# Optimization experiments

Measured on AMD Instinct MI355X. Metric: run time of the kernel, lower is better.

Reference implementation:

```python
import jax, jax.numpy as jnp
import numpy as np

NUM_HEADS = 16
GROUP_NUM = 4
HIDDEN = 1024
HEAD_DIM = HIDDEN // NUM_HEADS
EPS = 1e-5


def layernorm(x, g, b):
    mu = jnp.mean(x, axis=-1, keepdims=True)
    var = jnp.var(x, axis=-1, keepdims=True)
    return (x - mu) * jax.lax.rsqrt(var + EPS) * g + b


def setup_inputs() -> dict:
    key = jax.random.key(0)
    ks = jax.random.split(key, 12)
    s = 0.02
    return {
        "hidden_state": jax.random.normal(ks[0], (2, 2048, HIDDEN), jnp.float32),
        "wq": jax.random.normal(ks[1], (HIDDEN, HIDDEN), jnp.float32) * s,
        "bq": jnp.zeros((HIDDEN,), jnp.float32),
        "wk": jax.random.normal(ks[2], (GROUP_NUM * HEAD_DIM, HIDDEN), jnp.float32) * s,
        "bk": jnp.zeros((GROUP_NUM * HEAD_DIM,), jnp.float32),
        "wv": jax.random.normal(ks[3], (GROUP_NUM * HEAD_DIM, HIDDEN), jnp.float32) * s,
        "bv": jnp.zeros((GROUP_NUM * HEAD_DIM,), jnp.float32),
        "wo": jax.random.normal(ks[4], (HIDDEN, HIDDEN), jnp.float32) * s,
        "bo": jnp.zeros((HIDDEN,), jnp.float32),
        "ln_g": jnp.ones((HIDDEN,), jnp.float32),
        "ln_b": jnp.zeros((HIDDEN,), jnp.float32),
        "w1": jax.random.normal(ks[5], (HIDDEN, HIDDEN), jnp.float32) * s,
        "b1": jnp.zeros((HIDDEN,), jnp.float32),
        "w2": jax.random.normal(ks[6], (HIDDEN, HIDDEN), jnp.float32) * s,
        "b2": jnp.zeros((HIDDEN,), jnp.float32),
        "fln_g": jnp.ones((HIDDEN,), jnp.float32),
        "fln_b": jnp.zeros((HIDDEN,), jnp.float32),
    }


def reference(hidden_state, wq, bq, wk, bk, wv, bv, wo, bo, ln_g, ln_b,
              w1, b1, w2, b2, fln_g, fln_b):
    B, S, H = hidden_state.shape
    hpg = NUM_HEADS // GROUP_NUM  # heads per KV group

    q = hidden_state @ wq.T + bq  # [B,S,H]
    k = hidden_state @ wk.T + bk  # [B,S,G*D]
    v = hidden_state @ wv.T + bv

    q = q.reshape(B, S, NUM_HEADS, HEAD_DIM).transpose(0, 2, 1, 3)      # [B,Hh,S,D]
    k = k.reshape(B, S, GROUP_NUM, HEAD_DIM).transpose(0, 2, 1, 3)      # [B,G,S,D]
    v = v.reshape(B, S, GROUP_NUM, HEAD_DIM).transpose(0, 2, 1, 3)
    # expand KV groups to full head count (consecutive repeat, matching torch expand+reshape)
    k = jnp.repeat(k, hpg, axis=1)  # [B,Hh,S,D]
    v = jnp.repeat(v, hpg, axis=1)

    scale = 1.0 / jnp.sqrt(jnp.float32(HEAD_DIM))
    scores = jnp.einsum('bhsd,bhtd->bhst', q, k) * scale  # [B,Hh,S,S]
    probs = jax.nn.softmax(scores, axis=-1)
    attn = jnp.einsum('bhst,bhtd->bhsd', probs, v)  # [B,Hh,S,D]

    # Faithful to source: transpose(-1,-2) then raw flat view to [B, S, Hh*D]
    attn = jnp.swapaxes(attn, -1, -2).reshape(B, -1, HEAD_DIM * NUM_HEADS)

    out = layernorm(hidden_state + attn @ wo.T + bo, ln_g, ln_b)
    ffn = out @ w1.T + b1
    ffn = jax.nn.relu(ffn) @ w2.T + b2
    return layernorm(out + ffn, fln_g, fln_b)
```

## Files before the change

kernel.cpp:

```cpp
#include <hip/hip_runtime.h>
#include <math.h>

#define HIDDEN 1024
#define SEQ 2048

typedef __attribute__((ext_vector_type(8))) short short8;
typedef __attribute__((ext_vector_type(4))) float f32x4;

__device__ __forceinline__ unsigned short f2bf(float x) {
  union { float f; unsigned u; } c; c.f = x;
  unsigned r = c.u + 0x7FFFu + ((c.u >> 16) & 1u);
  return (unsigned short)(r >> 16);
}
__device__ __forceinline__ float bf2f(unsigned short h) {
  union { unsigned u; float f; } c; c.u = ((unsigned)h) << 16;
  return c.f;
}

__device__ __forceinline__ float fexp2(float x) {
  float r; asm("v_exp_f32 %0, %1" : "=v"(r) : "v"(x)); return r;
}

__device__ __forceinline__ unsigned cvt_pk_bf16(float lo, float hi) {
  unsigned r;
  asm("v_cvt_pk_bf16_f32 %0, %1, %2" : "=v"(r) : "v"(lo), "v"(hi));
  return r;
}

__device__ __forceinline__ void async_copy16(const void* g, void* l) {
  __builtin_amdgcn_global_load_lds(
      (const __attribute__((address_space(1))) unsigned int*)g,
      (__attribute__((address_space(3))) unsigned int*)l, 16, 0, 0);
}

__global__ __launch_bounds__(256) void cvt_all(
    const float* __restrict__ hs, const float* __restrict__ wq,
    const float* __restrict__ wk, const float* __restrict__ wv,
    const float* __restrict__ wo, const float* __restrict__ w1,
    const float* __restrict__ w2,
    unsigned short* __restrict__ hsb, unsigned short* __restrict__ wqb,
    unsigned short* __restrict__ wkb, unsigned short* __restrict__ wvb,
    unsigned short* __restrict__ wob, unsigned short* __restrict__ w1b,
    unsigned short* __restrict__ w2b)
{
  const int i = blockIdx.x * 256 + threadIdx.x;
  const float* src; unsigned short* dst; int off;
  if (i < 1048576)      { src = hs; dst = hsb; off = i; }
  else if (i < 1310720) { src = wq; dst = wqb; off = i - 1048576; }
  else if (i < 1376256) { src = wk; dst = wkb; off = i - 1310720; }
  else if (i < 1441792) { src = wv; dst = wvb; off = i - 1376256; }
  else if (i < 1703936) { src = wo; dst = wob; off = i - 1441792; }
  else if (i < 1966080) { src = w1; dst = w1b; off = i - 1703936; }
  else                  { src = w2; dst = w2b; off = i - 1966080; }
  float4 v = ((const float4*)src)[off];
  ushort4 o;
  o.x = f2bf(v.x); o.y = f2bf(v.y); o.z = f2bf(v.z); o.w = f2bf(v.w);
  ((ushort4*)dst)[off] = o;
}

template<bool RELU>
__global__ __launch_bounds__(256) void gemm_mfma(
    const unsigned short* __restrict__ A, const unsigned short* __restrict__ W,
    const float* __restrict__ bias, unsigned short* __restrict__ C,
    int M, int N, int K)
{
  __shared__ unsigned short As[64 * 64];
  __shared__ unsigned short Bs[64 * 64];
  const int tid = threadIdx.x;
  const int lane = tid & 63, wave = tid >> 6;
  const int ln = lane & 15, quad = lane >> 4;
  const int wm = (wave >> 1) * 32, wn = (wave & 1) * 32;

  const int flat = blockIdx.x;
  const int swz = (flat & 7) * ((int)gridDim.x >> 3) + (flat >> 3);
  const int ntx = N >> 6;
  const int m0 = (swz / ntx) * 64, n0 = (swz % ntx) * 64;

  f32x4 acc[2][2];
#pragma unroll
  for (int i = 0; i < 2; ++i)
#pragma unroll
    for (int j = 0; j < 2; ++j) acc[i][j] = (f32x4){0.f, 0.f, 0.f, 0.f};

  for (int k0 = 0; k0 < K; k0 += 64) {
#pragma unroll
    for (int it = 0; it < 2; ++it) {
      const int c = (wave * 2 + it) * 64 + lane;
      const int row = c >> 3, gc = (c & 7) ^ (row & 7);
      async_copy16(A + (size_t)(m0 + row) * K + k0 + gc * 8,
                   &As[(wave * 2 + it) * 512]);
      async_copy16(W + (size_t)(n0 + row) * K + k0 + gc * 8,
                   &Bs[(wave * 2 + it) * 512]);
    }
    __syncthreads();

    short8 af[2][2], bfr[2][2];
#pragma unroll
    for (int i = 0; i < 2; ++i) {
      const int row = wm + i * 16 + ln;
#pragma unroll
      for (int f = 0; f < 2; ++f) {
        const int ch = row * 8 + ((f * 4 + quad) ^ (row & 7));
        af[i][f] = *(const short8*)&As[ch * 8];
      }
    }
#pragma unroll
    for (int j = 0; j < 2; ++j) {
      const int row = wn + j * 16 + ln;
#pragma unroll
      for (int f = 0; f < 2; ++f) {
        const int ch = row * 8 + ((f * 4 + quad) ^ (row & 7));
        bfr[j][f] = *(const short8*)&Bs[ch * 8];
      }
    }
#pragma unroll
    for (int i = 0; i < 2; ++i)
#pragma unroll
      for (int j = 0; j < 2; ++j) {
        acc[i][j] = __builtin_amdgcn_mfma_f32_16x16x32_bf16(af[i][0], bfr[j][0], acc[i][j], 0, 0, 0);
        acc[i][j] = __builtin_amdgcn_mfma_f32_16x16x32_bf16(af[i][1], bfr[j][1], acc[i][j], 0, 0, 0);
      }
    __syncthreads();
  }

#pragma unroll
  for (int j = 0; j < 2; ++j) {
    const int n = n0 + wn + j * 16 + ln;
    const float bv = bias[n];
#pragma unroll
    for (int i = 0; i < 2; ++i) {
#pragma unroll
      for (int rr = 0; rr < 4; ++rr) {
        const int m = m0 + wm + i * 16 + quad * 4 + rr;
        float v = acc[i][j][rr] + bv;
        if (RELU) v = fmaxf(v, 0.f);
        C[(size_t)m * N + n] = f2bf(v);
      }
    }
  }
}

__global__ __launch_bounds__(256) void gemm_qkv(
    const unsigned short* __restrict__ A,
    const unsigned short* __restrict__ Wq, const unsigned short* __restrict__ Wk,
    const unsigned short* __restrict__ Wv,
    const float* __restrict__ bq, const float* __restrict__ bk,
    const float* __restrict__ bv,
    unsigned short* __restrict__ Qo, unsigned short* __restrict__ Ko,
    unsigned short* __restrict__ Vt)
{
  __shared__ unsigned short As[64 * 64];
  __shared__ unsigned short Bs[128 * 64];

  const int flat = blockIdx.x;
  const int swz = (flat & 7) * 96 + (flat >> 3);
  const int bx = swz % 12, by = swz / 12;

  int mode, nw0;
  const unsigned short* W;
  const float* bias;
  if (bx < 8)       { mode = 0; W = Wq; bias = bq; nw0 = bx * 128; }
  else if (bx < 10) { mode = 1; W = Wk; bias = bk; nw0 = (bx - 8) * 128; }
  else              { mode = 2; W = Wv; bias = bv; nw0 = (bx - 10) * 128; }

  const int tid = threadIdx.x;
  const int lane = tid & 63, wave = tid >> 6;
  const int ln = lane & 15, quad = lane >> 4;
  const int wm = (wave >> 1) * 32, wn = (wave & 1) * 64;
  const int m0 = by * 64;
  const int K = 1024;

  f32x4 acc[2][4];
#pragma unroll
  for (int i = 0; i < 2; ++i)
#pragma unroll
    for (int j = 0; j < 4; ++j) acc[i][j] = (f32x4){0.f, 0.f, 0.f, 0.f};

  for (int k0 = 0; k0 < K; k0 += 64) {
#pragma unroll
    for (int it = 0; it < 2; ++it) {
      const int c = (wave * 2 + it) * 64 + lane;
      const int row = c >> 3, gc = (c & 7) ^ (row & 7);
      async_copy16(A + (size_t)(m0 + row) * K + k0 + gc * 8,
                   &As[(wave * 2 + it) * 512]);
    }
#pragma unroll
    for (int it = 0; it < 4; ++it) {
      const int c = (wave * 4 + it) * 64 + lane;
      const int row = c >> 3, gc = (c & 7) ^ (row & 7);
      async_copy16(W + (size_t)(nw0 + row) * K + k0 + gc * 8,
                   &Bs[(wave * 4 + it) * 512]);
    }
    __syncthreads();

    short8 af[2][2], bfr[4][2];
#pragma unroll
    for (int i = 0; i < 2; ++i) {
      const int row = wm + i * 16 + ln;
#pragma unroll
      for (int f = 0; f < 2; ++f) {
        const int ch = row * 8 + ((f * 4 + quad) ^ (row & 7));
        af[i][f] = *(const short8*)&As[ch * 8];
      }
    }
#pragma unroll
    for (int j = 0; j < 4; ++j) {
      const int row = wn + j * 16 + ln;
#pragma unroll
      for (int f = 0; f < 2; ++f) {
        const int ch = row * 8 + ((f * 4 + quad) ^ (row & 7));
        bfr[j][f] = *(const short8*)&Bs[ch * 8];
      }
    }
#pragma unroll
    for (int i = 0; i < 2; ++i)
#pragma unroll
      for (int j = 0; j < 4; ++j) {
        acc[i][j] = __builtin_amdgcn_mfma_f32_16x16x32_bf16(af[i][0], bfr[j][0], acc[i][j], 0, 0, 0);
        acc[i][j] = __builtin_amdgcn_mfma_f32_16x16x32_bf16(af[i][1], bfr[j][1], acc[i][j], 0, 0, 0);
      }
    __syncthreads();
  }

#pragma unroll
  for (int j = 0; j < 4; ++j) {
    const int nl = nw0 + wn + j * 16 + ln;
    const float bvv = bias[nl];
#pragma unroll
    for (int i = 0; i < 2; ++i) {
#pragma unroll
      for (int rr = 0; rr < 4; ++rr) {
        const int m = m0 + wm + i * 16 + quad * 4 + rr;
        const float v = acc[i][j][rr] + bvv;
        if (mode == 0) {
          Qo[(size_t)m * 1024 + nl] = f2bf(v);
        } else if (mode == 1) {
          Ko[(size_t)m * 256 + nl] = f2bf(v);
        } else {
          const int b = m >> 11, s = m & 2047;
          Vt[((size_t)b * 256 + nl) * SEQ + s] = f2bf(v);
        }
      }
    }
  }
}

__global__ __launch_bounds__(256) void attn_mfma(
    const unsigned short* __restrict__ Q, const unsigned short* __restrict__ Kb,
    const unsigned short* __restrict__ Vt,
    unsigned short* __restrict__ N0, unsigned short* __restrict__ N1,
    float* __restrict__ LS)
{
  __shared__ unsigned short Ks[2][64 * 64];
  __shared__ unsigned short Vs[2][64 * 64];

  const int hwb = blockIdx.x;
  const int swz = (hwb & 7) * 64 + (hwb >> 3);
  const int qblk = swz & 7, half = (swz >> 3) & 1, h = (swz >> 4) & 15, b = swz >> 8;
  const int g = h >> 2;

  unsigned short* __restrict__ numO = half ? N1 : N0;
  float* __restrict__ lsO = LS + half * 65536;

  const int tid = threadIdx.x, lane = tid & 63, wave = tid >> 6;
  const int ln = lane & 15, quad = lane >> 4, q8 = quad * 8;
  const int s0 = qblk * 256;
  const float qscale = 0.125f * 1.44269504f;

  const int ln7 = ln & 7;
  const int x0 = (quad ^ ln7) * 8;
  const int x1 = ((4 + quad) ^ ln7) * 8;

  short8 ones;
#pragma unroll
  for (int e = 0; e < 8; ++e) ones[e] = (short)0x3F80;

  short8 qf[4][2];
#pragma unroll
  for (int qg = 0; qg < 4; ++qg) {
    const unsigned short* qsrc =
        Q + ((size_t)(b * SEQ + s0 + wave * 64 + qg * 16 + ln)) * 1024 + h * 64 + q8;
    qf[qg][0] = *(const short8*)qsrc;
    qf[qg][1] = *(const short8*)(qsrc + 32);
#pragma unroll
    for (int e = 0; e < 8; ++e) {
      qf[qg][0][e] = (short)f2bf(bf2f((unsigned short)qf[qg][0][e]) * qscale);
      qf[qg][1][e] = (short)f2bf(bf2f((unsigned short)qf[qg][1][e]) * qscale);
    }
  }

  const int srow = lane >> 3;
  const int sgcc = (lane & 7) ^ srow;

  auto stage = [&](int t0, int p) {
#pragma unroll
    for (int it = 0; it < 2; ++it) {
      const int row = wave * 16 + it * 8 + srow;
      const int skey = (row & 32) | ((row & 8) << 1) | ((row & 4) << 1) |
                       ((row & 16) >> 2) | (row & 3);
      async_copy16(Kb + (size_t)(b * SEQ + t0 + skey) * 256 + g * 64 + sgcc * 8,
                   &Ks[p][(wave * 2 + it) * 512]);
      async_copy16(Vt + (size_t)(b * 256 + g * 64 + row) * SEQ + t0 + sgcc * 8,
                   &Vs[p][(wave * 2 + it) * 512]);
    }
  };

  f32x4 of[4][4];
  f32x4 ls[4];
#pragma unroll
  for (int qg = 0; qg < 4; ++qg) {
    ls[qg] = (f32x4){0.f, 0.f, 0.f, 0.f};
#pragma unroll
    for (int jd = 0; jd < 4; ++jd) of[qg][jd] = (f32x4){0.f, 0.f, 0.f, 0.f};
  }

  const int tbase = half * 16;
  stage(tbase * 64, 0);

  for (int tt = 0; tt < 16; ++tt) {
    const int p = tt & 1;
    if (tt < 15) {
      stage((tbase + tt + 1) * 64, p ^ 1);
      asm volatile("s_waitcnt vmcnt(4)" ::: "memory");
    } else {
      asm volatile("s_waitcnt vmcnt(0)" ::: "memory");
    }
    __builtin_amdgcn_s_barrier();
    asm volatile("" ::: "memory");

    f32x4 sc[4][4];
#pragma unroll
    for (int jn = 0; jn < 4; ++jn) {
      const int krow = (jn * 16 + ln) * 64;
      const short8 kf0 = *(const short8*)&Ks[p][krow + x0];
      const short8 kf1 = *(const short8*)&Ks[p][krow + x1];
#pragma unroll
      for (int qg = 0; qg < 4; ++qg) {
        f32x4 z = (f32x4){0.f, 0.f, 0.f, 0.f};
        z = __builtin_amdgcn_mfma_f32_16x16x32_bf16(kf0, qf[qg][0], z, 0, 0, 0);
        z = __builtin_amdgcn_mfma_f32_16x16x32_bf16(kf1, qf[qg][1], z, 0, 0, 0);
        sc[qg][jn] = z;
      }
    }

    short8 pf[4][2];
#pragma unroll
    for (int qg = 0; qg < 4; ++qg) {
#pragma unroll
      for (int jn = 0; jn < 4; ++jn)
#pragma unroll
        for (int r = 0; r < 4; ++r) sc[qg][jn][r] = fexp2(sc[qg][jn][r]);
#pragma unroll
      for (int F = 0; F < 2; ++F) {
        union { unsigned u[4]; short8 s; } pk;
        pk.u[0] = cvt_pk_bf16(sc[qg][2 * F][0], sc[qg][2 * F][1]);
        pk.u[1] = cvt_pk_bf16(sc[qg][2 * F][2], sc[qg][2 * F][3]);
        pk.u[2] = cvt_pk_bf16(sc[qg][2 * F + 1][0], sc[qg][2 * F + 1][1]);
        pk.u[3] = cvt_pk_bf16(sc[qg][2 * F + 1][2], sc[qg][2 * F + 1][3]);
        pf[qg][F] = pk.s;
      }
      ls[qg] = __builtin_amdgcn_mfma_f32_16x16x32_bf16(pf[qg][0], ones, ls[qg], 0, 0, 0);
      ls[qg] = __builtin_amdgcn_mfma_f32_16x16x32_bf16(pf[qg][1], ones, ls[qg], 0, 0, 0);
    }

#pragma unroll
    for (int jd = 0; jd < 4; ++jd) {
      const int vrow = (jd * 16 + ln) * 64;
      const short8 vf0 = *(const short8*)&Vs[p][vrow + x0];
      const short8 vf1 = *(const short8*)&Vs[p][vrow + x1];
#pragma unroll
      for (int qg = 0; qg < 4; ++qg) {
        of[qg][jd] = __builtin_amdgcn_mfma_f32_16x16x32_bf16(pf[qg][0], vf0, of[qg][jd], 0, 0, 0);
        of[qg][jd] = __builtin_amdgcn_mfma_f32_16x16x32_bf16(pf[qg][1], vf1, of[qg][jd], 0, 0, 0);
      }
    }

    asm volatile("" ::: "memory");
    __builtin_amdgcn_s_barrier();
    asm volatile("" ::: "memory");
  }

#pragma unroll
  for (int qg = 0; qg < 4; ++qg) {
    const int sbase = s0 + wave * 64 + qg * 16 + quad * 4;
    if (ln == 0) {
#pragma unroll
      for (int r = 0; r < 4; ++r)
        lsO[(b * 16 + h) * 2048 + sbase + r] = ls[qg][r];
    }
#pragma unroll
    for (int jd = 0; jd < 4; ++jd) {
      const int d = jd * 16 + ln;
      ushort4 ov;
      ov.x = f2bf(of[qg][jd][0]);
      ov.y = f2bf(of[qg][jd][1]);
      ov.z = f2bf(of[qg][jd][2]);
      ov.w = f2bf(of[qg][jd][3]);
      *(ushort4*)&numO[((size_t)b * 1024 + h * 64 + d) * SEQ + sbase] = ov;
    }
  }
}

__global__ __launch_bounds__(256) void attn_reduce(
    const unsigned short* __restrict__ N0, unsigned short* att,
    const float* __restrict__ LS)
{
  const int i = (blockIdx.x * 256 + threadIdx.x) * 4;
  const int row = i >> 11, s = i & 2047;
  const int h = (row >> 6) & 15, b = row >> 10;
  const int lsi = (b * 16 + h) * 2048 + s;
  const float4 l0 = *(const float4*)&LS[lsi];
  const float4 l1 = *(const float4*)&LS[65536 + lsi];
  const ushort4 a = *(const ushort4*)&N0[i];
  const ushort4 c = *(const ushort4*)&att[i];
  ushort4 o;
  o.x = f2bf((bf2f(a.x) + bf2f(c.x)) / (l0.x + l1.x));
  o.y = f2bf((bf2f(a.y) + bf2f(c.y)) / (l0.y + l1.y));
  o.z = f2bf((bf2f(a.z) + bf2f(c.z)) / (l0.z + l1.z));
  o.w = f2bf((bf2f(a.w) + bf2f(c.w)) / (l0.w + l1.w));
  *(ushort4*)&att[i] = o;
}

__device__ __forceinline__ void ln_core(float x[4], const float* gam, const float* bet,
                                        int tid, float out[4]) {
  float s1 = x[0] + x[1] + x[2] + x[3];
  float s2 = x[0] * x[0] + x[1] * x[1] + x[2] * x[2] + x[3] * x[3];
#pragma unroll
  for (int off = 1; off < 64; off <<= 1) {
    s1 += __shfl_xor(s1, off);
    s2 += __shfl_xor(s2, off);
  }
  __shared__ float r1[4], r2[4];
  const int wave = tid >> 6;
  if ((tid & 63) == 0) { r1[wave] = s1; r2[wave] = s2; }
  __syncthreads();
  s1 = r1[0] + r1[1] + r1[2] + r1[3];
  s2 = r2[0] + r2[1] + r2[2] + r2[3];
  const float mu  = s1 * (1.0f / HIDDEN);
  const float var = s2 * (1.0f / HIDDEN) - mu * mu;
  const float inv = rsqrtf(var + 1e-5f);
  float4 gv = *(const float4*)&gam[tid * 4];
  float4 bv = *(const float4*)&bet[tid * 4];
  out[0] = (x[0] - mu) * inv * gv.x + bv.x;
  out[1] = (x[1] - mu) * inv * gv.y + bv.y;
  out[2] = (x[2] - mu) * inv * gv.z + bv.z;
  out[3] = (x[3] - mu) * inv * gv.w + bv.w;
}

__global__ __launch_bounds__(256) void resid_ln1(
    const float* __restrict__ X, const unsigned short* __restrict__ Y,
    const float* __restrict__ gam, const float* __restrict__ bet,
    unsigned short* __restrict__ outb)
{
  const int row = blockIdx.x, tid = threadIdx.x;
  const size_t base = (size_t)row * HIDDEN + tid * 4;
  float4 a = *(const float4*)&X[base];
  ushort4 yv = *(const ushort4*)&Y[base];
  float x[4] = {a.x + bf2f(yv.x), a.y + bf2f(yv.y), a.z + bf2f(yv.z), a.w + bf2f(yv.w)};
  float o[4];
  ln_core(x, gam, bet, tid, o);
  ushort4 ov;
  ov.x = f2bf(o[0]); ov.y = f2bf(o[1]); ov.z = f2bf(o[2]); ov.w = f2bf(o[3]);
  *(ushort4*)&outb[base] = ov;
}

__global__ __launch_bounds__(256) void resid_ln2(
    const unsigned short* __restrict__ X, const unsigned short* __restrict__ Y,
    const float* __restrict__ gam, const float* __restrict__ bet,
    float* __restrict__ out)
{
  const int row = blockIdx.x, tid = threadIdx.x;
  const size_t base = (size_t)row * HIDDEN + tid * 4;
  ushort4 xv = *(const ushort4*)&X[base];
  ushort4 yv = *(const ushort4*)&Y[base];
  float x[4] = {bf2f(xv.x) + bf2f(yv.x), bf2f(xv.y) + bf2f(yv.y),
                bf2f(xv.z) + bf2f(yv.z), bf2f(xv.w) + bf2f(yv.w)};
  float o[4];
  ln_core(x, gam, bet, tid, o);
  float4 ov; ov.x = o[0]; ov.y = o[1]; ov.z = o[2]; ov.w = o[3];
  *(float4*)&out[base] = ov;
}

extern "C" void kernel_launch(void* const* d_in, const int* in_sizes, int n_in,
                              void* d_out, int out_size, void* d_ws, size_t ws_size,
                              hipStream_t stream)
{
  (void)in_sizes; (void)n_in; (void)out_size; (void)ws_size;
  const float* hs  = (const float*)d_in[0];
  const float* wq  = (const float*)d_in[1];
  const float* bq  = (const float*)d_in[2];
  const float* wk  = (const float*)d_in[3];
  const float* bk  = (const float*)d_in[4];
  const float* wv  = (const float*)d_in[5];
  const float* bvp = (const float*)d_in[6];
  const float* wo  = (const float*)d_in[7];
  const float* bo  = (const float*)d_in[8];
  const float* lng = (const float*)d_in[9];
  const float* lnb = (const float*)d_in[10];
  const float* w1  = (const float*)d_in[11];
  const float* b1  = (const float*)d_in[12];
  const float* w2  = (const float*)d_in[13];
  const float* b2  = (const float*)d_in[14];
  const float* flg = (const float*)d_in[15];
  const float* flb = (const float*)d_in[16];
  float* out = (float*)d_out;

  unsigned short* w = (unsigned short*)d_ws;
  unsigned short* wqb = w;
  unsigned short* wkb = w + 1048576;
  unsigned short* wvb = w + 1310720;
  unsigned short* wob = w + 1572864;
  unsigned short* w1b = w + 2621440;
  unsigned short* w2b = w + 3670016;
  unsigned short* hsb = w + 4718592;
  unsigned short* qb  = w + 8912896;
  unsigned short* kb  = w + 13107200;
  unsigned short* vt  = w + 14155776;
  unsigned short* att = w + 15204352;
  unsigned short* f1b = hsb;
  unsigned short* yb  = qb;
  unsigned short* obb = att;
  unsigned short* f2b = qb;
  float* lsbuf = (float*)wqb;

  dim3 blk(256);
  cvt_all<<<dim3(8704), blk, 0, stream>>>(hs, wq, wk, wv, wo, w1, w2,
                                          hsb, wqb, wkb, wvb, wob, w1b, w2b);

  gemm_qkv<<<dim3(768), blk, 0, stream>>>(hsb, wqb, wkb, wvb, bq, bk, bvp,
                                          qb, kb, vt);
  attn_mfma<<<dim3(512), blk, 0, stream>>>(qb, kb, vt, hsb, att, lsbuf);
  attn_reduce<<<dim3(4096), blk, 0, stream>>>(hsb, att, lsbuf);
  gemm_mfma<false><<<dim3(1024), blk, 0, stream>>>(att, wob, bo, yb, 4096, 1024, 1024);
  resid_ln1<<<dim3(4096), blk, 0, stream>>>(hs, yb, lng, lnb, obb);
  gemm_mfma<true><<<dim3(1024), blk, 0, stream>>>(obb, w1b, b1, f1b, 4096, 1024, 1024);
  gemm_mfma<false><<<dim3(1024), blk, 0, stream>>>(f1b, w2b, b2, f2b, 4096, 1024, 1024);
  resid_ln2<<<dim3(4096), blk, 0, stream>>>(obb, f2b, flg, flb, out);
}
```

Measured before the change: 246.7 us.

## Use 128x128 double-buffered GEMM tiles and 8-wave attention blocks

The three dense GEMMs move from 64x64 tiles with 4 waves to 128x128 tiles with 8 waves, each wave computing a 64x32 subtile. Shared-memory tiles are now double-buffered, so the next K tile is prefetched while the current one is multiplied. Attention blocks double to 512 threads with each wave owning 32 query rows instead of 64, cutting per-wave registers to raise occupancy. The GEMM grid shrinks to 256 blocks, which may underfill the CUs, and the attention change adds more waves sharing each K/V tile.

```diff
diff --git a/kernel.cpp b/kernel.cpp
--- a/kernel.cpp
+++ b/kernel.cpp
@@ -59,49 +59,67 @@
 }
 
 template<bool RELU>
-__global__ __launch_bounds__(256) void gemm_mfma(
+__global__ __launch_bounds__(512) void gemm128(
     const unsigned short* __restrict__ A, const unsigned short* __restrict__ W,
     const float* __restrict__ bias, unsigned short* __restrict__ C,
     int M, int N, int K)
 {
-  __shared__ unsigned short As[64 * 64];
-  __shared__ unsigned short Bs[64 * 64];
+  __shared__ unsigned short As[2][128 * 64];
+  __shared__ unsigned short Bs[2][128 * 64];
   const int tid = threadIdx.x;
   const int lane = tid & 63, wave = tid >> 6;
   const int ln = lane & 15, quad = lane >> 4;
-  const int wm = (wave >> 1) * 32, wn = (wave & 1) * 32;
+  const int wm = (wave >> 2) * 64, wn = (wave & 3) * 32;
 
   const int flat = blockIdx.x;
   const int swz = (flat & 7) * ((int)gridDim.x >> 3) + (flat >> 3);
-  const int ntx = N >> 6;
-  const int m0 = (swz / ntx) * 64, n0 = (swz % ntx) * 64;
-
-  f32x4 acc[2][2];
-#pragma unroll
-  for (int i = 0; i < 2; ++i)
+  const int ntx = N >> 7;
+  const int m0 = (swz / ntx) * 128, n0 = (swz % ntx) * 128;
+
+  f32x4 acc[4][2];
+#pragma unroll
+  for (int i = 0; i < 4; ++i)
 #pragma unroll
     for (int j = 0; j < 2; ++j) acc[i][j] = (f32x4){0.f, 0.f, 0.f, 0.f};
 
-  for (int k0 = 0; k0 < K; k0 += 64) {
+  auto stage = [&](int k0, int p) {
 #pragma unroll
     for (int it = 0; it < 2; ++it) {
       const int c = (wave * 2 + it) * 64 + lane;
       const int row = c >> 3, gc = (c & 7) ^ (row & 7);
       async_copy16(A + (size_t)(m0 + row) * K + k0 + gc * 8,
-                   &As[(wave * 2 + it) * 512]);
+                   &As[p][(wave * 2 + it) * 512]);
+    }
+#pragma unroll
+    for (int it = 0; it < 2; ++it) {
+      const int c = (wave * 2 + it) * 64 + lane;
+      const int row = c >> 3, gc = (c & 7) ^ (row & 7);
       async_copy16(W + (size_t)(n0 + row) * K + k0 + gc * 8,
-                   &Bs[(wave * 2 + it) * 512]);
-    }
-    __syncthreads();
-
-    short8 af[2][2], bfr[2][2];
-#pragma unroll
-    for (int i = 0; i < 2; ++i) {
+                   &Bs[p][(wave * 2 + it) * 512]);
+    }
+  };
+
+  stage(0, 0);
+  const int NT = K >> 6;
+  for (int t = 0; t < NT; ++t) {
+    const int p = t & 1;
+    if (t < NT - 1) {
+      stage((t + 1) * 64, p ^ 1);
+      asm volatile("s_waitcnt vmcnt(4)" ::: "memory");
+    } else {
+      asm volatile("s_waitcnt vmcnt(0)" ::: "memory");
+    }
+    __builtin_amdgcn_s_barrier();
+    asm volatile("" ::: "memory");
+
+    short8 af[4][2], bfr[2][2];
+#pragma unroll
+    for (int i = 0; i < 4; ++i) {
       const int row = wm + i * 16 + ln;
 #pragma unroll
       for (int f = 0; f < 2; ++f) {
         const int ch = row * 8 + ((f * 4 + quad) ^ (row & 7));
-        af[i][f] = *(const short8*)&As[ch * 8];
+        af[i][f] = *(const short8*)&As[p][ch * 8];
       }
     }
 #pragma unroll
@@ -110,17 +128,20 @@
 #pragma unroll
       for (int f = 0; f < 2; ++f) {
         const int ch = row * 8 + ((f * 4 + quad) ^ (row & 7));
-        bfr[j][f] = *(const short8*)&Bs[ch * 8];
-      }
-    }
-#pragma unroll
-    for (int i = 0; i < 2; ++i)
+        bfr[j][f] = *(const short8*)&Bs[p][ch * 8];
+      }
+    }
+#pragma unroll
+    for (int i = 0; i < 4; ++i)
 #pragma unroll
       for (int j = 0; j < 2; ++j) {
         acc[i][j] = __builtin_amdgcn_mfma_f32_16x16x32_bf16(af[i][0], bfr[j][0], acc[i][j], 0, 0, 0);
         acc[i][j] = __builtin_amdgcn_mfma_f32_16x16x32_bf16(af[i][1], bfr[j][1], acc[i][j], 0, 0, 0);
       }
-    __syncthreads();
+
+    asm volatile("" ::: "memory");
+    __builtin_amdgcn_s_barrier();
+    asm volatile("" ::: "memory");
   }
 
 #pragma unroll
@@ -128,7 +149,7 @@
     const int n = n0 + wn + j * 16 + ln;
     const float bv = bias[n];
 #pragma unroll
-    for (int i = 0; i < 2; ++i) {
+    for (int i = 0; i < 4; ++i) {
 #pragma unroll
       for (int rr = 0; rr < 4; ++rr) {
         const int m = m0 + wm + i * 16 + quad * 4 + rr;
@@ -245,7 +266,7 @@
   }
 }
 
-__global__ __launch_bounds__(256) void attn_mfma(
+__global__ __launch_bounds__(512, 4) void attn_mfma(
     const unsigned short* __restrict__ Q, const unsigned short* __restrict__ Kb,
     const unsigned short* __restrict__ Vt,
     unsigned short* __restrict__ N0, unsigned short* __restrict__ N1,
@@ -275,11 +296,11 @@
 #pragma unroll
   for (int e = 0; e < 8; ++e) ones[e] = (short)0x3F80;
 
-  short8 qf[4][2];
-#pragma unroll
-  for (int qg = 0; qg < 4; ++qg) {
+  short8 qf[2][2];
+#pragma unroll
+  for (int qg = 0; qg < 2; ++qg) {
     const unsigned short* qsrc =
-        Q + ((size_t)(b * SEQ + s0 + wave * 64 + qg * 16 + ln)) * 1024 + h * 64 + q8;
+        Q + ((size_t)(b * SEQ + s0 + wave * 32 + qg * 16 + ln)) * 1024 + h * 64 + q8;
     qf[qg][0] = *(const short8*)qsrc;
     qf[qg][1] = *(const short8*)(qsrc + 32);
 #pragma unroll
@@ -293,22 +314,19 @@
   const int sgcc = (lane & 7) ^ srow;
 
   auto stage = [&](int t0, int p) {
-#pragma unroll
-    for (int it = 0; it < 2; ++it) {
-      const int row = wave * 16 + it * 8 + srow;
-      const int skey = (row & 32) | ((row & 8) << 1) | ((row & 4) << 1) |
-                       ((row & 16) >> 2) | (row & 3);
-      async_copy16(Kb + (size_t)(b * SEQ + t0 + skey) * 256 + g * 64 + sgcc * 8,
-                   &Ks[p][(wave * 2 + it) * 512]);
-      async_copy16(Vt + (size_t)(b * 256 + g * 64 + row) * SEQ + t0 + sgcc * 8,
-                   &Vs[p][(wave * 2 + it) * 512]);
-    }
+    const int row = wave * 8 + srow;
+    const int skey = (row & 32) | ((row & 8) << 1) | ((row & 4) << 1) |
+                     ((row & 16) >> 2) | (row & 3);
+    async_copy16(Kb + (size_t)(b * SEQ + t0 + skey) * 256 + g * 64 + sgcc * 8,
+                 &Ks[p][wave * 512]);
+    async_copy16(Vt + (size_t)(b * 256 + g * 64 + row) * SEQ + t0 + sgcc * 8,
+                 &Vs[p][wave * 512]);
   };
 
-  f32x4 of[4][4];
-  f32x4 ls[4];
-#pragma unroll
-  for (int qg = 0; qg < 4; ++qg) {
+  f32x4 of[2][4];
+  f32x4 ls[2];
+#pragma unroll
+  for (int qg = 0; qg < 2; ++qg) {
     ls[qg] = (f32x4){0.f, 0.f, 0.f, 0.f};
 #pragma unroll
     for (int jd = 0; jd < 4; ++jd) of[qg][jd] = (f32x4){0.f, 0.f, 0.f, 0.f};
@@ -321,21 +339,21 @@
     const int p = tt & 1;
     if (tt < 15) {
       stage((tbase + tt + 1) * 64, p ^ 1);
-      asm volatile("s_waitcnt vmcnt(4)" ::: "memory");
+      asm volatile("s_waitcnt vmcnt(2)" ::: "memory");
     } else {
       asm volatile("s_waitcnt vmcnt(0)" ::: "memory");
     }
     __builtin_amdgcn_s_barrier();
     asm volatile("" ::: "memory");
 
-    f32x4 sc[4][4];
+    f32x4 sc[2][4];
 #pragma unroll
     for (int jn = 0; jn < 4; ++jn) {
       const int krow = (jn * 16 + ln) * 64;
       const short8 kf0 = *(const short8*)&Ks[p][krow + x0];
       const short8 kf1 = *(const short8*)&Ks[p][krow + x1];
 #pragma unroll
-      for (int qg = 0; qg < 4; ++qg) {
+      for (int qg = 0; qg < 2; ++qg) {
         f32x4 z = (f32x4){0.f, 0.f, 0.f, 0.f};
         z = __builtin_amdgcn_mfma_f32_16x16x32_bf16(kf0, qf[qg][0], z, 0, 0, 0);
         z = __builtin_amdgcn_mfma_f32_16x16x32_bf16(kf1, qf[qg][1], z, 0, 0, 0);
@@ -343,9 +361,9 @@
       }
     }
 
-    short8 pf[4][2];
-#pragma unroll
-    for (int qg = 0; qg < 4; ++qg) {
+    short8 pf[2][2];
+#pragma unroll
+    for (int qg = 0; qg < 2; ++qg) {
 #pragma unroll
       for (int jn = 0; jn < 4; ++jn)
 #pragma unroll
@@ -369,7 +387,7 @@
       const short8 vf0 = *(const short8*)&Vs[p][vrow + x0];
       const short8 vf1 = *(const short8*)&Vs[p][vrow + x1];
 #pragma unroll
-      for (int qg = 0; qg < 4; ++qg) {
+      for (int qg = 0; qg < 2; ++qg) {
         of[qg][jd] = __builtin_amdgcn_mfma_f32_16x16x32_bf16(pf[qg][0], vf0, of[qg][jd], 0, 0, 0);
         of[qg][jd] = __builtin_amdgcn_mfma_f32_16x16x32_bf16(pf[qg][1], vf1, of[qg][jd], 0, 0, 0);
       }
@@ -381,8 +399,8 @@
   }
 
 #pragma unroll
-  for (int qg = 0; qg < 4; ++qg) {
-    const int sbase = s0 + wave * 64 + qg * 16 + quad * 4;
+  for (int qg = 0; qg < 2; ++qg) {
+    const int sbase = s0 + wave * 32 + qg * 16 + quad * 4;
     if (ln == 0) {
 #pragma unroll
       for (int r = 0; r < 4; ++r)
@@ -529,11 +547,11 @@
 
   gemm_qkv<<<dim3(768), blk, 0, stream>>>(hsb, wqb, wkb, wvb, bq, bk, bvp,
                                           qb, kb, vt);
-  attn_mfma<<<dim3(512), blk, 0, stream>>>(qb, kb, vt, hsb, att, lsbuf);
+  attn_mfma<<<dim3(512), dim3(512), 0, stream>>>(qb, kb, vt, hsb, att, lsbuf);
   attn_reduce<<<dim3(4096), blk, 0, stream>>>(hsb, att, lsbuf);
-  gemm_mfma<false><<<dim3(1024), blk, 0, stream>>>(att, wob, bo, yb, 4096, 1024, 1024);
+  gemm128<false><<<dim3(256), dim3(512), 0, stream>>>(att, wob, bo, yb, 4096, 1024, 1024);
   resid_ln1<<<dim3(4096), blk, 0, stream>>>(hs, yb, lng, lnb, obb);
-  gemm_mfma<true><<<dim3(1024), blk, 0, stream>>>(obb, w1b, b1, f1b, 4096, 1024, 1024);
-  gemm_mfma<false><<<dim3(1024), blk, 0, stream>>>(f1b, w2b, b2, f2b, 4096, 1024, 1024);
+  gemm128<true><<<dim3(256), dim3(512), 0, stream>>>(obb, w1b, b1, f1b, 4096, 1024, 1024);
+  gemm128<false><<<dim3(256), dim3(512), 0, stream>>>(f1b, w2b, b2, f2b, 4096, 1024, 1024);
   resid_ln2<<<dim3(4096), blk, 0, stream>>>(obb, f2b, flg, flb, out);
 }
```

New measurement: 236.0 us. 1.05x faster.
